# Optimization experiments

Hardware: AMD Instinct MI355X
Metric: run time of the kernel (lower is better)

## Reference

```python
import jax, jax.numpy as jnp
import numpy as np

B, K, N, M = 32, 128, 128, 256  # batch, num_classes(==n_dim), n_dim, samples-per-matrix
EPSILON = 0.1
LAMBDA_SOFTMAX = 0.1
LEARNING_RATE = 0.01
BN_EPS = 1e-5


def setup_inputs() -> dict:
    key = jax.random.key(0)
    k1, k2, k3 = jax.random.split(key, 3)
    x = jax.random.normal(k1, (B, N, M), dtype=jnp.float32)
    A = jax.random.normal(k2, (K, N, N), dtype=jnp.float32) * 0.1
    EC_proto = jnp.einsum('kij,klj->kil', A, A)  # per-class PSD prototype covariances (K,N,N)
    EC_count = jax.random.uniform(k3, (K,), dtype=jnp.float32, minval=1.0, maxval=100.0)
    return {"x": x, "EC_proto": EC_proto, "EC_count": EC_count}


def reference(x, EC_proto, EC_count):
    n = x.shape[1]
    dtype = x.dtype
    # BatchNorm1d(num_classes, affine=False, track_running_stats=False): batch stats over (N, L)
    mean = x.mean(axis=(0, 2), keepdims=True)
    var = x.var(axis=(0, 2), keepdims=True)  # biased variance, as torch uses for normalization
    x = (x - mean) / jnp.sqrt(var + BN_EPS)

    eye = jnp.eye(n, dtype=dtype)
    total = EC_count.sum()
    has_counts = total > 1e-6

    # E branch: global expansion operator
    e_alpha = jnp.where(has_counts, n / (EPSILON * EPSILON * total), jnp.zeros((), dtype))
    e = e_alpha * jnp.linalg.inv(e_alpha * EC_proto.sum(0) + eye)  # (N,N)
    e_x_z = jnp.einsum('ij,bjm->bim', e, x)  # (B,N,M)

    # C branch: per-class compression operators
    bool_depth = (EC_count != 0).astype(dtype)  # (K,)
    count_fix = EC_count + (1.0 - bool_depth)
    c_alpha = (n / (count_fix * EPSILON * EPSILON) * bool_depth)[:, None, None]  # (K,1,1)
    c = c_alpha * jnp.linalg.inv(c_alpha * EC_proto + eye[None])  # (K,N,N)
    c_x_z = jnp.einsum('kij,bjm->bkim', c, x)  # (B,K,N,M)

    # Frobenius norm per (b,k), rescaled to sum to 10 over classes
    norm = jnp.sqrt((c_x_z * c_x_z).sum(axis=(2, 3)))  # (B,K)
    norm = 10.0 * norm / norm.sum(axis=1, keepdims=True)

    pi = jax.nn.softmax(-LAMBDA_SOFTMAX * norm, axis=1) * bool_depth  # (B,K)
    gama = jnp.where(has_counts, EC_count / total, jnp.zeros_like(EC_count))  # (K,)

    z_d = e_x_z - jnp.einsum('k,bkim,bk->bim', gama, c_x_z, pi)  # (B,N,M)
    return x + LEARNING_RATE * z_d
```

## Files before the change

### kernel.cpp

```cpp
#include <hip/hip_runtime.h>
#include <math.h>

#define Bb 32
#define Kk 128
#define Nn 128
#define Mm 256
#define EPS2 0.01f
#define LAMBDA_S 0.1f
#define LR 0.01f
#define BN_EPS_C 1e-5f

#define SWZ(c) (((c) & 14) | (((c) & 1) << 4) | (((c) >> 4) & 1))

__global__ void kA_bn_psum(const float* __restrict__ x, const float* __restrict__ P,
                           float* __restrict__ xn, float* __restrict__ Psum) {
  int t = threadIdx.x;
  if (blockIdx.x < 128) {
    int n = blockIdx.x;
    float s = 0.f, s2 = 0.f;
    #pragma unroll 4
    for (int b = 0; b < Bb; ++b) {
      float v = x[(size_t)b * (Nn * Mm) + n * Mm + t];
      s += v;
      s2 += v * v;
    }
    #pragma unroll
    for (int o = 32; o > 0; o >>= 1) {
      s += __shfl_down(s, o, 64);
      s2 += __shfl_down(s2, o, 64);
    }
    __shared__ float rs[4], rs2[4];
    if ((t & 63) == 0) { rs[t >> 6] = s; rs2[t >> 6] = s2; }
    __syncthreads();
    float S = rs[0] + rs[1] + rs[2] + rs[3];
    float S2 = rs2[0] + rs2[1] + rs2[2] + rs2[3];
    float mean = S * (1.0f / (Bb * Mm));
    float var = S2 * (1.0f / (Bb * Mm)) - mean * mean;
    float rstd = 1.0f / sqrtf(var + BN_EPS_C);
    #pragma unroll 4
    for (int b = 0; b < Bb; ++b) {
      size_t idx = (size_t)b * (Nn * Mm) + n * Mm + t;
      xn[idx] = (x[idx] - mean) * rstd;
    }
  } else {
    int e = (blockIdx.x - 128) * 256 + t;
    float s = 0.f;
    #pragma unroll 8
    for (int k = 0; k < Kk; ++k) s += P[(size_t)k * 16384 + e];
    Psum[e] = s;
  }
}

__global__ __launch_bounds__(256, 1) void k3S(
    const float* __restrict__ P, const float* __restrict__ Psum,
    const float* __restrict__ cnt, float* __restrict__ C,
    const float* __restrict__ xn, float* __restrict__ S) {
  __shared__ __align__(16) float LB[8448];
  int bx = blockIdx.x;
  int t = threadIdx.x;

  if (bx < 129) {
    float* Mt = LB;
    float* Rb = LB + 2112;
    float* redc = LB + 4160;
    int blk = bx;
    int tx = t & 15, ty = t >> 4;

    float cv = cnt[t & 127];
    float sr = cv;
    #pragma unroll
    for (int o = 32; o > 0; o >>= 1) sr += __shfl_down(sr, o, 64);
    if ((t & 63) == 0) redc[t >> 6] = sr;
    __syncthreads();
    float total = redc[0] + redc[1];
    bool has = total > 1e-6f;
    float av;
    if (blk < 128) {
      float c = cnt[blk];
      float bk = (c != 0.0f) ? 1.0f : 0.0f;
      float cfix = c + (1.0f - bk);
      av = (float)Nn / (cfix * EPS2) * bk;
    } else {
      av = has ? ((float)Nn / (EPS2 * total)) : 0.0f;
    }
    const float* src = (blk < 128) ? (P + (size_t)blk * 16384) : Psum;

    float a[8][8];
    #pragma unroll
    for (int i = 0; i < 8; ++i) {
      int row = ty * 8 + i;
      float4 p0 = *(const float4*)&src[row * 128 + tx * 8];
      float4 p1 = *(const float4*)&src[row * 128 + tx * 8 + 4];
      a[i][0] = av * p0.x; a[i][1] = av * p0.y; a[i][2] = av * p0.z; a[i][3] = av * p0.w;
      a[i][4] = av * p1.x; a[i][5] = av * p1.y; a[i][6] = av * p1.z; a[i][7] = av * p1.w;
      if (tx == ty) a[i][i] += 1.0f;
    }

    for (int kb = 0; kb < 8; ++kb) {
      int k0 = kb * 16;
      if ((ty >> 1) == kb) {
        int d = ty & 1;
        #pragma unroll
        for (int i = 0; i < 8; ++i) {
          *(float4*)&Rb[(d * 8 + i) * 128 + SWZ(2 * tx) * 4] =
              make_float4(a[i][0], a[i][1], a[i][2], a[i][3]);
          *(float4*)&Rb[(d * 8 + i) * 128 + SWZ(2 * tx + 1) * 4] =
              make_float4(a[i][4], a[i][5], a[i][6], a[i][7]);
        }
      }
      if ((tx >> 1) == kb) {
        int dh = tx & 1;
        #pragma unroll
        for (int i = 0; i < 8; ++i)
          #pragma unroll
          for (int j = 0; j < 8; ++j)
            Mt[(dh * 8 + j) * 132 + ty * 8 + i] = a[i][j];
      }
      __syncthreads();

      if (t < 64) {
        int l = t;
        float m[2][16];
        #pragma unroll
        for (int d = 0; d < 2; ++d)
          #pragma unroll
          for (int j = 0; j < 16; ++j)
            m[d][j] = Mt[j * 132 + 2 * l + d];
        #pragma unroll
        for (int q = 0; q < 16; ++q) {
          int lq = (k0 + q) >> 1;
          float pr[16];
          #pragma unroll
          for (int j = 0; j < 16; ++j) pr[j] = __shfl(m[q & 1][j], lq, 64);
          float pinv = 1.0f / pr[q];
          #pragma unroll
          for (int d = 0; d < 2; ++d) {
            float f = m[d][q];
            bool isp = (2 * l + d == k0 + q);
            float g = isp ? (1.0f - pinv) : f * pinv;
            #pragma unroll
            for (int j = 0; j < 16; ++j) m[d][j] = fmaf(-g, pr[j], m[d][j]);
            m[d][q] = isp ? pinv : -g;
          }
        }
        #pragma unroll
        for (int d = 0; d < 2; ++d)
          #pragma unroll
          for (int j = 0; j < 16; ++j)
            Mt[j * 132 + 2 * l + d] = m[d][j];
      }
      __syncthreads();

      if ((ty >> 1) == kb) {
        #pragma unroll
        for (int i = 0; i < 8; ++i)
          #pragma unroll
          for (int j = 0; j < 8; ++j) a[i][j] = 0.0f;
      }
      #pragma unroll
      for (int q = 0; q < 16; ++q) {
        float4 m0 = *(const float4*)&Mt[q * 132 + ty * 8];
        float4 m1 = *(const float4*)&Mt[q * 132 + ty * 8 + 4];
        float4 r0 = *(const float4*)&Rb[q * 128 + SWZ(2 * tx) * 4];
        float4 r1 = *(const float4*)&Rb[q * 128 + SWZ(2 * tx + 1) * 4];
        float mq[8] = {m0.x, m0.y, m0.z, m0.w, m1.x, m1.y, m1.z, m1.w};
        float rq[8] = {r0.x, r0.y, r0.z, r0.w, r1.x, r1.y, r1.z, r1.w};
        #pragma unroll
        for (int i = 0; i < 8; ++i)
          #pragma unroll
          for (int j = 0; j < 8; ++j)
            a[i][j] = fmaf(mq[i], rq[j], a[i][j]);
      }
      if ((tx >> 1) == kb) {
        int dh = tx & 1;
        #pragma unroll
        for (int j = 0; j < 8; ++j) {
          float4 v0 = *(const float4*)&Mt[(dh * 8 + j) * 132 + ty * 8];
          float4 v1 = *(const float4*)&Mt[(dh * 8 + j) * 132 + ty * 8 + 4];
          a[0][j] = v0.x; a[1][j] = v0.y; a[2][j] = v0.z; a[3][j] = v0.w;
          a[4][j] = v1.x; a[5][j] = v1.y; a[6][j] = v1.z; a[7][j] = v1.w;
        }
      }
      __syncthreads();
    }

    float* dst = C + (size_t)blk * 16384;
    #pragma unroll
    for (int i = 0; i < 8; ++i) {
      int row = ty * 8 + i;
      float4 v0 = make_float4(av * a[i][0], av * a[i][1], av * a[i][2], av * a[i][3]);
      float4 v1 = make_float4(av * a[i][4], av * a[i][5], av * a[i][6], av * a[i][7]);
      *(float4*)&dst[row * 128 + tx * 8] = v0;
      *(float4*)&dst[row * 128 + tx * 8 + 4] = v1;
    }
  } else {
    int bxx = bx - 129;
    int b = bxx >> 1;
    int jbase = (bxx & 1) * 64;
    float* X = LB;
    int tx = t & 15, ty = t >> 4;
    float acc[8][4] = {};
    for (int mc = 0; mc < Mm; mc += 64) {
      __syncthreads();
      for (int c = 0; c < 32; ++c) {
        int e = c * 256 + t;
        int i = e >> 6, mm = e & 63;
        X[i * 65 + mm] = xn[(size_t)b * (Nn * Mm) + i * Mm + mc + mm];
      }
      __syncthreads();
      for (int mm = 0; mm < 64; ++mm) {
        float ai[8], bj[4];
        #pragma unroll
        for (int q = 0; q < 8; ++q) ai[q] = X[(ty * 8 + q) * 65 + mm];
        #pragma unroll
        for (int q = 0; q < 4; ++q) bj[q] = X[(jbase + tx * 4 + q) * 65 + mm];
        #pragma unroll
        for (int qi = 0; qi < 8; ++qi)
          #pragma unroll
          for (int qj = 0; qj < 4; ++qj)
            acc[qi][qj] = fmaf(ai[qi], bj[qj], acc[qi][qj]);
      }
    }
    float* dst = S + (size_t)b * 16384;
    #pragma unroll
    for (int qi = 0; qi < 8; ++qi) {
      float4 v = make_float4(acc[qi][0], acc[qi][1], acc[qi][2], acc[qi][3]);
      *(float4*)&dst[(ty * 8 + qi) * 128 + jbase + tx * 4] = v;
    }
  }
}

__global__ __launch_bounds__(256, 1) void kGN(const float* __restrict__ C,
                                              const float* __restrict__ S,
                                              float* __restrict__ norm2h) {
  __shared__ __align__(16) float LB[128 * 128];
  __shared__ float redb[4][32];
  int k = blockIdx.x >> 1, h = blockIdx.x & 1;
  int t = threadIdx.x;
  const float* src = C + (size_t)k * 16384;
  for (int c = 0; c < 64; ++c) LB[c * 256 + t] = src[c * 256 + t];
  __syncthreads();
  int tx = t & 15, ty = t >> 4;
  int i0 = ty * 8, j0 = h * 64 + tx * 4;
  float acc[8][4] = {};
  for (int l = 0; l < 128; ++l) {
    float ai[8], bj[4];
    *(float4*)&ai[0] = *(const float4*)&LB[l * 128 + i0];
    *(float4*)&ai[4] = *(const float4*)&LB[l * 128 + i0 + 4];
    *(float4*)&bj[0] = *(const float4*)&LB[l * 128 + j0];
    #pragma unroll
    for (int qi = 0; qi < 8; ++qi)
      #pragma unroll
      for (int qj = 0; qj < 4; ++qj)
        acc[qi][qj] = fmaf(ai[qi], bj[qj], acc[qi][qj]);
  }
  __syncthreads();
  #pragma unroll
  for (int qi = 0; qi < 8; ++qi)
    *(float4*)&LB[(i0 + qi) * 64 + tx * 4] =
        make_float4(acc[qi][0], acc[qi][1], acc[qi][2], acc[qi][3]);
  __syncthreads();
  float nacc[32];
  #pragma unroll
  for (int b = 0; b < 32; ++b) nacc[b] = 0.0f;
  #pragma unroll
  for (int q = 0; q < 8; ++q) {
    int el = (q * 256 + t) * 4;
    float4 g = *(const float4*)&LB[el];
    int i = el >> 6, jl = el & 63;
    const float* sb = S + i * 128 + h * 64 + jl;
    #pragma unroll
    for (int b = 0; b < 32; ++b) {
      float4 sv = *(const float4*)&sb[(size_t)b * 16384];
      nacc[b] = fmaf(g.x, sv.x, nacc[b]);
      nacc[b] = fmaf(g.y, sv.y, nacc[b]);
      nacc[b] = fmaf(g.z, sv.z, nacc[b]);
      nacc[b] = fmaf(g.w, sv.w, nacc[b]);
    }
  }
  #pragma unroll
  for (int b = 0; b < 32; ++b) {
    float v = nacc[b];
    #pragma unroll
    for (int o = 32; o > 0; o >>= 1) v += __shfl_down(v, o, 64);
    nacc[b] = v;
  }
  if ((t & 63) == 0) {
    int w = t >> 6;
    #pragma unroll
    for (int b = 0; b < 32; ++b) redb[w][b] = nacc[b];
  }
  __syncthreads();
  if (t < 32)
    norm2h[(size_t)k * 64 + h * 32 + t] =
        redb[0][t] + redb[1][t] + redb[2][t] + redb[3][t];
}

__global__ void k7n(const float* __restrict__ norm2h, const float* __restrict__ cnt,
                    float* __restrict__ wT) {
  int b = blockIdx.x;
  int k = threadIdx.x;
  float n2 = norm2h[(size_t)k * 64 + b] + norm2h[(size_t)k * 64 + 32 + b];
  float norm = sqrtf(fmaxf(n2, 0.0f));
  float cv = cnt[k];
  __shared__ float r1[2], r2[2], r3[2];
  float tt = cv, r = norm;
  #pragma unroll
  for (int o = 32; o > 0; o >>= 1) {
    tt += __shfl_down(tt, o, 64);
    r += __shfl_down(r, o, 64);
  }
  if ((k & 63) == 0) { r1[k >> 6] = tt; r2[k >> 6] = r; }
  __syncthreads();
  float total = r1[0] + r1[1];
  float sumn = r2[0] + r2[1];
  float nr = 10.0f * norm / fmaxf(sumn, 1e-30f);
  float ex = expf(-LAMBDA_S * nr);
  float e2 = ex;
  #pragma unroll
  for (int o = 32; o > 0; o >>= 1) e2 += __shfl_down(e2, o, 64);
  if ((k & 63) == 0) r3[k >> 6] = e2;
  __syncthreads();
  float sume = r3[0] + r3[1];
  float bk = (cv != 0.0f) ? 1.0f : 0.0f;
  float pi = (ex / sume) * bk;
  float gama = (total > 1e-6f) ? (cv / total) : 0.0f;
  wT[k * 32 + b] = gama * pi;
}

__global__ __launch_bounds__(256, 1) void k8_k(const float* __restrict__ C,
                                               const float* __restrict__ E,
                                               const float* __restrict__ wT,
                                               float* __restrict__ F) {
  int e = blockIdx.x * 256 + threadIdx.x;
  int b0 = blockIdx.y * 8;
  float acc[8];
  float ev = E[e];
  #pragma unroll
  for (int b = 0; b < 8; ++b) acc[b] = ev;
  for (int k = 0; k < 128; ++k) {
    float cv = C[(size_t)k * 16384 + e];
    const float* wk = wT + k * 32 + b0;
    #pragma unroll
    for (int b = 0; b < 8; ++b) acc[b] = fmaf(-wk[b], cv, acc[b]);
  }
  #pragma unroll
  for (int b = 0; b < 8; ++b) F[(size_t)(b0 + b) * 16384 + e] = acc[b];
}

__global__ __launch_bounds__(256, 1) void k9_k(const float* __restrict__ F,
                                               const float* __restrict__ xn,
                                               float* __restrict__ out) {
  int bx = blockIdx.x;
  int b = bx >> 3, y = bx & 7;
  int mq = y >> 1, ih = y & 1;
  __shared__ __align__(16) float Ft[64 * 68];
  __shared__ __align__(16) float Xt[64 * 68];
  int t = threadIdx.x;
  int tx = t & 15, ty = t >> 4;
  float acc[4][4] = {};
  for (int jc = 0; jc < 128; jc += 64) {
    __syncthreads();
    #pragma unroll
    for (int q = 0; q < 4; ++q) {
      int e = q * 256 + t;
      int i = e >> 4, j4 = e & 15;
      *(float4*)&Ft[i * 68 + j4 * 4] =
          *(const float4*)&F[(size_t)b * 16384 + (ih * 64 + i) * 128 + jc + j4 * 4];
    }
    #pragma unroll
    for (int q = 0; q < 4; ++q) {
      int e = q * 256 + t;
      int jj = e >> 4, m4 = e & 15;
      *(float4*)&Xt[jj * 68 + m4 * 4] =
          *(const float4*)&xn[(size_t)b * (Nn * Mm) + (jc + jj) * Mm + mq * 64 + m4 * 4];
    }
    __syncthreads();
    for (int j4 = 0; j4 < 16; ++j4) {
      float4 fi[4], xm[4];
      #pragma unroll
      for (int r = 0; r < 4; ++r)
        fi[r] = *(const float4*)&Ft[(ty * 4 + r) * 68 + j4 * 4];
      #pragma unroll
      for (int r = 0; r < 4; ++r)
        xm[r] = *(const float4*)&Xt[(j4 * 4 + r) * 68 + tx * 4];
      #pragma unroll
      for (int qi = 0; qi < 4; ++qi) {
        #pragma unroll
        for (int qm = 0; qm < 4; ++qm) {
          float xv = ((const float*)&xm[0])[qm];
          acc[qi][qm] = fmaf(fi[qi].x, xv, acc[qi][qm]);
          xv = ((const float*)&xm[1])[qm];
          acc[qi][qm] = fmaf(fi[qi].y, xv, acc[qi][qm]);
          xv = ((const float*)&xm[2])[qm];
          acc[qi][qm] = fmaf(fi[qi].z, xv, acc[qi][qm]);
          xv = ((const float*)&xm[3])[qm];
          acc[qi][qm] = fmaf(fi[qi].w, xv, acc[qi][qm]);
        }
      }
    }
  }
  int i0 = ih * 64 + ty * 4, m0 = mq * 64 + tx * 4;
  #pragma unroll
  for (int qi = 0; qi < 4; ++qi) {
    float4 xv = *(const float4*)&xn[(size_t)b * (Nn * Mm) + (i0 + qi) * Mm + m0];
    float4 o;
    o.x = fmaf(LR, acc[qi][0], xv.x);
    o.y = fmaf(LR, acc[qi][1], xv.y);
    o.z = fmaf(LR, acc[qi][2], xv.z);
    o.w = fmaf(LR, acc[qi][3], xv.w);
    *(float4*)&out[(size_t)b * (Nn * Mm) + (i0 + qi) * Mm + m0] = o;
  }
}

extern "C" void kernel_launch(void* const* d_in, const int* in_sizes, int n_in,
                              void* d_out, int out_size, void* d_ws, size_t ws_size,
                              hipStream_t stream) {
  const float* x = (const float*)d_in[0];
  const float* P = (const float*)d_in[1];
  const float* cnt = (const float*)d_in[2];
  float* out = (float*)d_out;

  float* ws = (float*)d_ws;
  float* xn = ws;
  float* C = xn + 1048576;
  float* S = C + 2113536;
  float* norm2h = S + 524288;
  float* wT = norm2h + 8192;
  float* F = wT + 4096;
  float* Psum = F + 524288;
  size_t need_bytes = (size_t)((Psum + 16384) - ws) * sizeof(float);
  if (ws_size < need_bytes) return;

  hipLaunchKernelGGL(kA_bn_psum, dim3(192), dim3(256), 0, stream, x, P, xn, Psum);
  hipLaunchKernelGGL(k3S, dim3(193), dim3(256), 0, stream, P, Psum, cnt, C, xn, S);
  hipLaunchKernelGGL(kGN, dim3(256), dim3(256), 0, stream, C, S, norm2h);
  hipLaunchKernelGGL(k7n, dim3(32), dim3(128), 0, stream, norm2h, cnt, wT);
  hipLaunchKernelGGL(k8_k, dim3(64, 4), dim3(256), 0, stream, C,
                     C + (size_t)128 * 16384, wT, F);
  hipLaunchKernelGGL(k9_k, dim3(256), dim3(256), 0, stream, F, xn, out);
}
```

Measured before the change: 169.3 us.

## Double k3S block size to 512 threads and cache BN inputs in registers

The matrix-inversion and Gram kernel k3S now runs with 512 threads per block. Each thread holds a 4x8 slice instead of 8x8, and the Gram part handles one full batch matrix per block, so the grid shrinks to 161 blocks. The pivot broadcast now uses readlane, and the pivot reciprocal uses a hardware rcp plus one Newton step. The BatchNorm kernel keeps all 32 loaded values in registers so x is not read a second time. The aim is to shorten the serial Gauss-Jordan critical path through more parallelism and cheaper per-pivot operations, at the cost of more register pressure and a slightly less exact reciprocal.

```diff
diff --git a/kernel.cpp b/kernel.cpp
--- a/kernel.cpp
+++ b/kernel.cpp
@@ -12,17 +12,22 @@
 
 #define SWZ(c) (((c) & 14) | (((c) & 1) << 4) | (((c) >> 4) & 1))
 
+__device__ __forceinline__ float readlane_f(float v, int lane) {
+  return __int_as_float(__builtin_amdgcn_readlane(__float_as_int(v), lane));
+}
+
 __global__ void kA_bn_psum(const float* __restrict__ x, const float* __restrict__ P,
                            float* __restrict__ xn, float* __restrict__ Psum) {
   int t = threadIdx.x;
   if (blockIdx.x < 128) {
     int n = blockIdx.x;
+    float v[32];
     float s = 0.f, s2 = 0.f;
-    #pragma unroll 4
+    #pragma unroll
     for (int b = 0; b < Bb; ++b) {
-      float v = x[(size_t)b * (Nn * Mm) + n * Mm + t];
-      s += v;
-      s2 += v * v;
+      v[b] = x[(size_t)b * (Nn * Mm) + n * Mm + t];
+      s += v[b];
+      s2 += v[b] * v[b];
     }
     #pragma unroll
     for (int o = 32; o > 0; o >>= 1) {
@@ -37,11 +42,9 @@
     float mean = S * (1.0f / (Bb * Mm));
     float var = S2 * (1.0f / (Bb * Mm)) - mean * mean;
     float rstd = 1.0f / sqrtf(var + BN_EPS_C);
-    #pragma unroll 4
-    for (int b = 0; b < Bb; ++b) {
-      size_t idx = (size_t)b * (Nn * Mm) + n * Mm + t;
-      xn[idx] = (x[idx] - mean) * rstd;
-    }
+    #pragma unroll
+    for (int b = 0; b < Bb; ++b)
+      xn[(size_t)b * (Nn * Mm) + n * Mm + t] = (v[b] - mean) * rstd;
   } else {
     int e = (blockIdx.x - 128) * 256 + t;
     float s = 0.f;
@@ -51,7 +54,7 @@
   }
 }
 
-__global__ __launch_bounds__(256, 1) void k3S(
+__global__ __launch_bounds__(512, 1) void k3S(
     const float* __restrict__ P, const float* __restrict__ Psum,
     const float* __restrict__ cnt, float* __restrict__ C,
     const float* __restrict__ xn, float* __restrict__ S) {
@@ -64,13 +67,14 @@
     float* Rb = LB + 2112;
     float* redc = LB + 4160;
     int blk = bx;
-    int tx = t & 15, ty = t >> 4;
+    int tx = t & 15;
+    int ty = t >> 4;
 
     float cv = cnt[t & 127];
     float sr = cv;
     #pragma unroll
     for (int o = 32; o > 0; o >>= 1) sr += __shfl_down(sr, o, 64);
-    if ((t & 63) == 0) redc[t >> 6] = sr;
+    if ((t & 63) == 0 && t < 128) redc[t >> 6] = sr;
     __syncthreads();
     float total = redc[0] + redc[1];
     bool has = total > 1e-6f;
@@ -85,36 +89,35 @@
     }
     const float* src = (blk < 128) ? (P + (size_t)blk * 16384) : Psum;
 
-    float a[8][8];
-    #pragma unroll
-    for (int i = 0; i < 8; ++i) {
-      int row = ty * 8 + i;
+    float a[4][8];
+    #pragma unroll
+    for (int i = 0; i < 4; ++i) {
+      int row = ty * 4 + i;
       float4 p0 = *(const float4*)&src[row * 128 + tx * 8];
       float4 p1 = *(const float4*)&src[row * 128 + tx * 8 + 4];
       a[i][0] = av * p0.x; a[i][1] = av * p0.y; a[i][2] = av * p0.z; a[i][3] = av * p0.w;
       a[i][4] = av * p1.x; a[i][5] = av * p1.y; a[i][6] = av * p1.z; a[i][7] = av * p1.w;
-      if (tx == ty) a[i][i] += 1.0f;
+      if (tx == (ty >> 1)) a[i][(ty & 1) * 4 + i] += 1.0f;
     }
 
     for (int kb = 0; kb < 8; ++kb) {
       int k0 = kb * 16;
-      if ((ty >> 1) == kb) {
-        int d = ty & 1;
-        #pragma unroll
-        for (int i = 0; i < 8; ++i) {
-          *(float4*)&Rb[(d * 8 + i) * 128 + SWZ(2 * tx) * 4] =
+      if ((ty >> 2) == kb) {
+        int d = (ty & 3) * 4;
+        #pragma unroll
+        for (int i = 0; i < 4; ++i) {
+          *(float4*)&Rb[(d + i) * 128 + SWZ(2 * tx) * 4] =
               make_float4(a[i][0], a[i][1], a[i][2], a[i][3]);
-          *(float4*)&Rb[(d * 8 + i) * 128 + SWZ(2 * tx + 1) * 4] =
+          *(float4*)&Rb[(d + i) * 128 + SWZ(2 * tx + 1) * 4] =
               make_float4(a[i][4], a[i][5], a[i][6], a[i][7]);
         }
       }
       if ((tx >> 1) == kb) {
         int dh = tx & 1;
         #pragma unroll
-        for (int i = 0; i < 8; ++i)
-          #pragma unroll
-          for (int j = 0; j < 8; ++j)
-            Mt[(dh * 8 + j) * 132 + ty * 8 + i] = a[i][j];
+        for (int j = 0; j < 8; ++j)
+          *(float4*)&Mt[(dh * 8 + j) * 132 + ty * 4] =
+              make_float4(a[0][j], a[1][j], a[2][j], a[3][j]);
       }
       __syncthreads();
 
@@ -131,8 +134,10 @@
           int lq = (k0 + q) >> 1;
           float pr[16];
           #pragma unroll
-          for (int j = 0; j < 16; ++j) pr[j] = __shfl(m[q & 1][j], lq, 64);
-          float pinv = 1.0f / pr[q];
+          for (int j = 0; j < 16; ++j) pr[j] = readlane_f(m[q & 1][j], lq);
+          float piv = pr[q];
+          float r0 = __builtin_amdgcn_rcpf(piv);
+          float pinv = r0 * (2.0f - piv * r0);
           #pragma unroll
           for (int d = 0; d < 2; ++d) {
             float f = m[d][q];
@@ -151,22 +156,21 @@
       }
       __syncthreads();
 
-      if ((ty >> 1) == kb) {
-        #pragma unroll
-        for (int i = 0; i < 8; ++i)
+      if ((ty >> 2) == kb) {
+        #pragma unroll
+        for (int i = 0; i < 4; ++i)
           #pragma unroll
           for (int j = 0; j < 8; ++j) a[i][j] = 0.0f;
       }
       #pragma unroll
       for (int q = 0; q < 16; ++q) {
-        float4 m0 = *(const float4*)&Mt[q * 132 + ty * 8];
-        float4 m1 = *(const float4*)&Mt[q * 132 + ty * 8 + 4];
-        float4 r0 = *(const float4*)&Rb[q * 128 + SWZ(2 * tx) * 4];
-        float4 r1 = *(const float4*)&Rb[q * 128 + SWZ(2 * tx + 1) * 4];
-        float mq[8] = {m0.x, m0.y, m0.z, m0.w, m1.x, m1.y, m1.z, m1.w};
-        float rq[8] = {r0.x, r0.y, r0.z, r0.w, r1.x, r1.y, r1.z, r1.w};
-        #pragma unroll
-        for (int i = 0; i < 8; ++i)
+        float4 mq4 = *(const float4*)&Mt[q * 132 + ty * 4];
+        float4 r0q = *(const float4*)&Rb[q * 128 + SWZ(2 * tx) * 4];
+        float4 r1q = *(const float4*)&Rb[q * 128 + SWZ(2 * tx + 1) * 4];
+        float mq[4] = {mq4.x, mq4.y, mq4.z, mq4.w};
+        float rq[8] = {r0q.x, r0q.y, r0q.z, r0q.w, r1q.x, r1q.y, r1q.z, r1q.w};
+        #pragma unroll
+        for (int i = 0; i < 4; ++i)
           #pragma unroll
           for (int j = 0; j < 8; ++j)
             a[i][j] = fmaf(mq[i], rq[j], a[i][j]);
@@ -175,10 +179,8 @@
         int dh = tx & 1;
         #pragma unroll
         for (int j = 0; j < 8; ++j) {
-          float4 v0 = *(const float4*)&Mt[(dh * 8 + j) * 132 + ty * 8];
-          float4 v1 = *(const float4*)&Mt[(dh * 8 + j) * 132 + ty * 8 + 4];
-          a[0][j] = v0.x; a[1][j] = v0.y; a[2][j] = v0.z; a[3][j] = v0.w;
-          a[4][j] = v1.x; a[5][j] = v1.y; a[6][j] = v1.z; a[7][j] = v1.w;
+          float4 v = *(const float4*)&Mt[(dh * 8 + j) * 132 + ty * 4];
+          a[0][j] = v.x; a[1][j] = v.y; a[2][j] = v.z; a[3][j] = v.w;
         }
       }
       __syncthreads();
@@ -186,46 +188,47 @@
 
     float* dst = C + (size_t)blk * 16384;
     #pragma unroll
-    for (int i = 0; i < 8; ++i) {
-      int row = ty * 8 + i;
+    for (int i = 0; i < 4; ++i) {
+      int row = ty * 4 + i;
       float4 v0 = make_float4(av * a[i][0], av * a[i][1], av * a[i][2], av * a[i][3]);
       float4 v1 = make_float4(av * a[i][4], av * a[i][5], av * a[i][6], av * a[i][7]);
       *(float4*)&dst[row * 128 + tx * 8] = v0;
       *(float4*)&dst[row * 128 + tx * 8 + 4] = v1;
     }
   } else {
-    int bxx = bx - 129;
-    int b = bxx >> 1;
-    int jbase = (bxx & 1) * 64;
+    int b = bx - 129;
     float* X = LB;
     int tx = t & 15, ty = t >> 4;
-    float acc[8][4] = {};
+    float acc[4][8] = {};
     for (int mc = 0; mc < Mm; mc += 64) {
       __syncthreads();
-      for (int c = 0; c < 32; ++c) {
-        int e = c * 256 + t;
+      #pragma unroll
+      for (int c = 0; c < 16; ++c) {
+        int e = c * 512 + t;
         int i = e >> 6, mm = e & 63;
         X[i * 65 + mm] = xn[(size_t)b * (Nn * Mm) + i * Mm + mc + mm];
       }
       __syncthreads();
       for (int mm = 0; mm < 64; ++mm) {
-        float ai[8], bj[4];
-        #pragma unroll
-        for (int q = 0; q < 8; ++q) ai[q] = X[(ty * 8 + q) * 65 + mm];
-        #pragma unroll
-        for (int q = 0; q < 4; ++q) bj[q] = X[(jbase + tx * 4 + q) * 65 + mm];
-        #pragma unroll
-        for (int qi = 0; qi < 8; ++qi)
-          #pragma unroll
-          for (int qj = 0; qj < 4; ++qj)
+        float ai[4], bj[8];
+        #pragma unroll
+        for (int q = 0; q < 4; ++q) ai[q] = X[(ty * 4 + q) * 65 + mm];
+        #pragma unroll
+        for (int q = 0; q < 8; ++q) bj[q] = X[(tx * 8 + q) * 65 + mm];
+        #pragma unroll
+        for (int qi = 0; qi < 4; ++qi)
+          #pragma unroll
+          for (int qj = 0; qj < 8; ++qj)
             acc[qi][qj] = fmaf(ai[qi], bj[qj], acc[qi][qj]);
       }
     }
     float* dst = S + (size_t)b * 16384;
     #pragma unroll
-    for (int qi = 0; qi < 8; ++qi) {
-      float4 v = make_float4(acc[qi][0], acc[qi][1], acc[qi][2], acc[qi][3]);
-      *(float4*)&dst[(ty * 8 + qi) * 128 + jbase + tx * 4] = v;
+    for (int qi = 0; qi < 4; ++qi) {
+      *(float4*)&dst[(ty * 4 + qi) * 128 + tx * 8] =
+          make_float4(acc[qi][0], acc[qi][1], acc[qi][2], acc[qi][3]);
+      *(float4*)&dst[(ty * 4 + qi) * 128 + tx * 8 + 4] =
+          make_float4(acc[qi][4], acc[qi][5], acc[qi][6], acc[qi][7]);
     }
   }
 }
@@ -433,7 +436,7 @@
   if (ws_size < need_bytes) return;
 
   hipLaunchKernelGGL(kA_bn_psum, dim3(192), dim3(256), 0, stream, x, P, xn, Psum);
-  hipLaunchKernelGGL(k3S, dim3(193), dim3(256), 0, stream, P, Psum, cnt, C, xn, S);
+  hipLaunchKernelGGL(k3S, dim3(161), dim3(512), 0, stream, P, Psum, cnt, C, xn, S);
   hipLaunchKernelGGL(kGN, dim3(256), dim3(256), 0, stream, C, S, norm2h);
   hipLaunchKernelGGL(k7n, dim3(32), dim3(128), 0, stream, norm2h, cnt, wT);
   hipLaunchKernelGGL(k8_k, dim3(64, 4), dim3(256), 0, stream, C,
```

Result: slower. 173.9 us (+2.7%).
